# Performance work log

Measured on AMD Instinct MI355X. Metric: run time of the kernel, lower is better.

Reference implementation:

```python
import jax, jax.numpy as jnp
import numpy as np

R = 16                      # grid resolution per axis -> R**3 = 4096 experts
E = R ** 3
L_XYZ = 10                  # xyz positional-encoding frequencies -> input_ch = 63
L_DIR = 4                   # dir positional-encoding frequencies -> input_ch_views = 27
HID = 32                    # KiloNeRF W
AABB_MIN = -1.5
AABB_MAX = 1.5


def posenc(x, L):
    # NeRF positional encoding: [x, sin(2^l x), cos(2^l x)] for l in 0..L-1
    freqs = 2.0 ** jnp.arange(L, dtype=x.dtype)          # (L,)
    xb = x[..., None, :] * freqs[:, None]                # (..., L, 3)
    enc = jnp.concatenate([jnp.sin(xb), jnp.cos(xb)], axis=-1)  # (..., L, 6)
    return jnp.concatenate([x, enc.reshape(x.shape[:-1] + (-1,))], axis=-1)


def _linear_init(key, shape, fan_in):
    s = 1.0 / np.sqrt(fan_in)
    return jax.random.uniform(key, shape, jnp.float32, -s, s)


def setup_inputs() -> dict:
    key = jax.random.key(0)
    ks = jax.random.split(key, 16)
    in_pts = 3 + 6 * L_XYZ     # 63
    in_dirs = 3 + 6 * L_DIR    # 27
    in_view = in_dirs + HID    # 59
    return {
        "pts": jax.random.normal(ks[0], (1024, 64, 3), jnp.float32),
        "viewdirs": jax.random.normal(ks[1], (1024, 3), jnp.float32),
        "W1": _linear_init(ks[2], (E, in_pts, HID), in_pts),
        "b1": _linear_init(ks[3], (E, HID), in_pts),
        "W2": _linear_init(ks[4], (E, HID, HID), HID),
        "b2": _linear_init(ks[5], (E, HID), HID),
        "Wf": _linear_init(ks[6], (E, HID, HID), HID),
        "bf": _linear_init(ks[7], (E, HID), HID),
        "Wsig": _linear_init(ks[8], (E, HID, 1), HID),
        "bsig": _linear_init(ks[9], (E, 1), HID),
        "Wv": _linear_init(ks[10], (E, in_view, HID), in_view),
        "bv": _linear_init(ks[11], (E, HID), in_view),
        "Wrgb": _linear_init(ks[12], (E, HID, 3), HID),
        "brgb": _linear_init(ks[13], (E, 3), HID),
    }


def reference(pts, viewdirs, W1, b1, W2, b2, Wf, bf, Wsig, bsig, Wv, bv, Wrgb, brgb):
    N_rays, N_samples, _ = pts.shape
    p = pts.reshape(-1, 3)                                           # (N,3)
    d = jnp.broadcast_to(viewdirs[:, None, :], (N_rays, N_samples, 3)).reshape(-1, 3)

    # voxel index per point (Network._get_index)
    norm = (p - AABB_MIN) / (AABB_MAX - AABB_MIN)
    scaled = jnp.clip(norm * R, 0.0, R - 1.0)
    idx = scaled.astype(jnp.int32)                                   # (N,3)
    e = idx[:, 0] * (R * R) + idx[:, 1] * R + idx[:, 2]              # (N,) expert id

    xp = posenc(p, L_XYZ)                                            # (N,63)
    xd = posenc(d, L_DIR)                                            # (N,27)

    # grouped tiny-MLP dispatch, vectorized as per-point gathered weights
    h = jax.nn.relu(jnp.einsum('ni,nio->no', xp, W1[e]) + b1[e])     # (N,32)
    h = jax.nn.relu(jnp.einsum('ni,nio->no', h, W2[e]) + b2[e])      # (N,32)
    sigma = jnp.einsum('ni,nio->no', h, Wsig[e]) + bsig[e]           # (N,1)
    feat = jnp.einsum('ni,nio->no', h, Wf[e]) + bf[e]                # (N,32)
    hv = jnp.concatenate([feat, xd], axis=-1)                        # (N,59)
    hv = jax.nn.relu(jnp.einsum('ni,nio->no', hv, Wv[e]) + bv[e])    # (N,32)
    rgb = jnp.einsum('ni,nio->no', hv, Wrgb[e]) + brgb[e]            # (N,3)

    return rgb.reshape(N_rays, N_samples, 3), sigma.reshape(N_rays, N_samples, 1)
```

## Files before the change

### kernel.cpp

```cpp
#include <hip/hip_runtime.h>


#define WS_COUNTS 0
#define WS_OFFSETS 4096
#define WS_CURSOR 8192
#define WS_ORDER 12288

#define L_W1 0
#define L_W2 2016
#define L_WF 3040
#define L_WV 4064
#define L_WS 5952
#define L_WR 5984
#define L_B1 6080
#define L_B2 6112
#define L_BF 6144
#define L_BV 6176
#define L_BSR 6208
#define L_TOT 6212

__device__ __forceinline__ int expert_id(float px, float py, float pz) {
    float nx = (px - (-1.5f)) / 3.0f;
    float ny = (py - (-1.5f)) / 3.0f;
    float nz = (pz - (-1.5f)) / 3.0f;
    float sx = fminf(fmaxf(nx * 16.0f, 0.0f), 15.0f);
    float sy = fminf(fmaxf(ny * 16.0f, 0.0f), 15.0f);
    float sz = fminf(fmaxf(nz * 16.0f, 0.0f), 15.0f);
    return (int)sx * 256 + (int)sy * 16 + (int)sz;
}

template <int N4>
__device__ __forceinline__ void stage256(float* dst, const float* __restrict__ src,
                                         int tid) {
    constexpr int ITER = (N4 + 255) / 256;
    float4 buf[ITER];
#pragma unroll
    for (int j = 0; j < ITER; ++j) {
        const int t = j * 256 + tid;
        if (t < N4) buf[j] = ((const float4*)src)[t];
    }
#pragma unroll
    for (int j = 0; j < ITER; ++j) {
        const int t = j * 256 + tid;
        if (t < N4) ((float4*)dst)[t] = buf[j];
    }
}

__device__ __forceinline__ float enc_val(int idx, float x, float y, float z) {
    if (idx < 3) return (idx == 0) ? x : ((idx == 1) ? y : z);
    const int k = idx - 3;
    const int l = k / 6;
    const int r = k - 6 * l;
    const int c = (r < 3) ? r : r - 3;
    const float cv = (c == 0) ? x : ((c == 1) ? y : z);
    const float a = ldexpf(cv, l);
    return (r < 3) ? sinf(a) : cosf(a);
}

__global__ __launch_bounds__(256) void hist_kernel(const float* __restrict__ pts,
                                                   int* __restrict__ counts, int n) {
    int i = blockIdx.x * 256 + threadIdx.x;
    if (i < n) {
        int e = expert_id(pts[3 * i + 0], pts[3 * i + 1], pts[3 * i + 2]);
        atomicAdd(&counts[e], 1);
    }
}

__global__ __launch_bounds__(256) void scan_kernel(const int* __restrict__ counts,
                                                   int* __restrict__ offsets,
                                                   int* __restrict__ cursor) {
    const int tid = threadIdx.x;
    const int lane = tid & 63, wave = tid >> 6;
    const int base = tid * 16;
    int c[16], loc[16], sum = 0;
#pragma unroll
    for (int j = 0; j < 16; ++j) c[j] = counts[base + j];
#pragma unroll
    for (int j = 0; j < 16; ++j) { loc[j] = sum; sum += c[j]; }
    int v = sum;
#pragma unroll
    for (int off = 1; off <= 32; off <<= 1) {
        int u = __shfl_up(v, off, 64);
        if (lane >= off) v += u;
    }
    __shared__ int wtot[4];
    if (lane == 63) wtot[wave] = v;
    __syncthreads();
    int wbase = 0;
    for (int w = 0; w < wave; ++w) wbase += wtot[w];
    const int excl = wbase + v - sum;
#pragma unroll
    for (int j = 0; j < 16; ++j) {
        int o = excl + loc[j];
        offsets[base + j] = o;
        cursor[base + j] = o;
    }
}

__global__ __launch_bounds__(256) void scatter_kernel(const float* __restrict__ pts,
                                                      int* __restrict__ cursor,
                                                      int* __restrict__ order, int n) {
    int i = blockIdx.x * 256 + threadIdx.x;
    if (i < n) {
        int e = expert_id(pts[3 * i + 0], pts[3 * i + 1], pts[3 * i + 2]);
        int pos = atomicAdd(&cursor[e], 1);
        order[pos] = i;
    }
}

__global__ __launch_bounds__(256) void expert_mlp_kernel(
    const float* __restrict__ pts, const float* __restrict__ viewdirs,
    const float* __restrict__ W1, const float* __restrict__ b1,
    const float* __restrict__ W2, const float* __restrict__ b2,
    const float* __restrict__ Wf, const float* __restrict__ bfc,
    const float* __restrict__ Wsig, const float* __restrict__ bsig,
    const float* __restrict__ Wv, const float* __restrict__ bv,
    const float* __restrict__ Wrgb, const float* __restrict__ brgb,
    const int* __restrict__ counts, const int* __restrict__ offsets,
    const int* __restrict__ order,
    float* __restrict__ out_rgb, float* __restrict__ out_sigma, int samples) {

    const int e = blockIdx.x;
    const int cnt = counts[e];
    if (cnt == 0) return;
    const int start = offsets[e];
    const int tid = threadIdx.x;
    const int wave = tid >> 6;
    const int lane = tid & 63;
    const int h = lane >> 5;
    const int o = lane & 31;

    __shared__ float lw[L_TOT];
    __shared__ float xs[4][4][64];
    __shared__ float xd[4][4][32];

    stage256<504>(lw + L_W1, W1 + (size_t)e * 2016, tid);
    stage256<256>(lw + L_W2, W2 + (size_t)e * 1024, tid);
    stage256<256>(lw + L_WF, Wf + (size_t)e * 1024, tid);
    stage256<472>(lw + L_WV, Wv + (size_t)e * 1888, tid);
    stage256<8>(lw + L_WS, Wsig + (size_t)e * 32, tid);
    stage256<24>(lw + L_WR, Wrgb + (size_t)e * 96, tid);
    stage256<8>(lw + L_B1, b1 + (size_t)e * 32, tid);
    stage256<8>(lw + L_B2, b2 + (size_t)e * 32, tid);
    stage256<8>(lw + L_BF, bfc + (size_t)e * 32, tid);
    stage256<8>(lw + L_BV, bv + (size_t)e * 32, tid);
    if (tid == 0) lw[L_BSR] = bsig[e];
    if (tid < 3) lw[L_BSR + 1 + tid] = brgb[3 * e + tid];
    __syncthreads();

    const float b1o = lw[L_B1 + o];
    const float b2o = lw[L_B2 + o];
    const float bfo = lw[L_BF + o];
    const float bvo = lw[L_BV + o];
    const float wsg = lw[L_WS + o];
    const float wr0 = lw[L_WR + 3 * o + 0];
    const float wr1 = lw[L_WR + 3 * o + 1];
    const float wr2 = lw[L_WR + 3 * o + 2];
    const float bsg = lw[L_BSR];
    const float br0 = lw[L_BSR + 1], br1 = lw[L_BSR + 2], br2 = lw[L_BSR + 3];

    float* xsA = xs[wave][h];     float* xsB = xs[wave][2 + h];
    float* xdA = xd[wave][h];     float* xdB = xd[wave][2 + h];

    const bool pow2 = (samples & (samples - 1)) == 0;
    const int sh = 31 - __clz(samples);

    for (int s0 = 4 * wave; s0 < cnt; s0 += 16) {
        const int sA = s0 + h, sB = s0 + 2 + h;
        const bool liveA = (sA < cnt), liveB = (sB < cnt);
        const int ptA = order[start + (liveA ? sA : cnt - 1)];
        const int ptB = order[start + (liveB ? sB : cnt - 1)];

        const float pxA = pts[3 * ptA + 0], pyA = pts[3 * ptA + 1], pzA = pts[3 * ptA + 2];
        const float pxB = pts[3 * ptB + 0], pyB = pts[3 * ptB + 1], pzB = pts[3 * ptB + 2];
        const int rayA = pow2 ? (ptA >> sh) : (ptA / samples);
        const int rayB = pow2 ? (ptB >> sh) : (ptB / samples);
        const float dxA = viewdirs[3 * rayA + 0], dyA = viewdirs[3 * rayA + 1], dzA = viewdirs[3 * rayA + 2];
        const float dxB = viewdirs[3 * rayB + 0], dyB = viewdirs[3 * rayB + 1], dzB = viewdirs[3 * rayB + 2];

        xsA[o] = enc_val(o, pxA, pyA, pzA);
        xsB[o] = enc_val(o, pxB, pyB, pzB);
        if (o < 31) {
            xsA[o + 32] = enc_val(o + 32, pxA, pyA, pzA);
            xsB[o + 32] = enc_val(o + 32, pxB, pyB, pzB);
        }
        if (o < 27) {
            xdA[o] = enc_val(o, dxA, dyA, dzA);
            xdB[o] = enc_val(o, dxB, dyB, dzB);
        }

        float aA = b1o, aB = b1o;
#pragma unroll
        for (int q = 0; q < 15; ++q) {
            const float w0 = lw[L_W1 + (4 * q + 0) * 32 + o];
            const float w1 = lw[L_W1 + (4 * q + 1) * 32 + o];
            const float w2 = lw[L_W1 + (4 * q + 2) * 32 + o];
            const float w3 = lw[L_W1 + (4 * q + 3) * 32 + o];
            const float4 xA = *(const float4*)&xsA[4 * q];
            const float4 xB = *(const float4*)&xsB[4 * q];
            aA = fmaf(xA.x, w0, aA); aB = fmaf(xB.x, w0, aB);
            aA = fmaf(xA.y, w1, aA); aB = fmaf(xB.y, w1, aB);
            aA = fmaf(xA.z, w2, aA); aB = fmaf(xB.z, w2, aB);
            aA = fmaf(xA.w, w3, aA); aB = fmaf(xB.w, w3, aB);
        }
#pragma unroll
        for (int i = 60; i < 63; ++i) {
            const float w = lw[L_W1 + i * 32 + o];
            aA = fmaf(xsA[i], w, aA); aB = fmaf(xsB[i], w, aB);
        }
        xsA[o] = fmaxf(aA, 0.f);
        xsB[o] = fmaxf(aB, 0.f);

        aA = b2o; aB = b2o;
#pragma unroll
        for (int q = 0; q < 8; ++q) {
            const float w0 = lw[L_W2 + (4 * q + 0) * 32 + o];
            const float w1 = lw[L_W2 + (4 * q + 1) * 32 + o];
            const float w2 = lw[L_W2 + (4 * q + 2) * 32 + o];
            const float w3 = lw[L_W2 + (4 * q + 3) * 32 + o];
            const float4 xA = *(const float4*)&xsA[4 * q];
            const float4 xB = *(const float4*)&xsB[4 * q];
            aA = fmaf(xA.x, w0, aA); aB = fmaf(xB.x, w0, aB);
            aA = fmaf(xA.y, w1, aA); aB = fmaf(xB.y, w1, aB);
            aA = fmaf(xA.z, w2, aA); aB = fmaf(xB.z, w2, aB);
            aA = fmaf(xA.w, w3, aA); aB = fmaf(xB.w, w3, aB);
        }
        const float gA = fmaxf(aA, 0.f), gB = fmaxf(aB, 0.f);

        {
            float spA = gA * wsg, spB = gB * wsg;
#pragma unroll
            for (int m = 1; m <= 16; m <<= 1) {
                spA += __shfl_xor(spA, m, 64);
                spB += __shfl_xor(spB, m, 64);
            }
            if (liveA && o == 0) out_sigma[ptA] = spA + bsg;
            if (liveB && o == 0) out_sigma[ptB] = spB + bsg;
        }
        xsA[o] = gA;
        xsB[o] = gB;

        aA = bfo; aB = bfo;
#pragma unroll
        for (int q = 0; q < 8; ++q) {
            const float w0 = lw[L_WF + (4 * q + 0) * 32 + o];
            const float w1 = lw[L_WF + (4 * q + 1) * 32 + o];
            const float w2 = lw[L_WF + (4 * q + 2) * 32 + o];
            const float w3 = lw[L_WF + (4 * q + 3) * 32 + o];
            const float4 xA = *(const float4*)&xsA[4 * q];
            const float4 xB = *(const float4*)&xsB[4 * q];
            aA = fmaf(xA.x, w0, aA); aB = fmaf(xB.x, w0, aB);
            aA = fmaf(xA.y, w1, aA); aB = fmaf(xB.y, w1, aB);
            aA = fmaf(xA.z, w2, aA); aB = fmaf(xB.z, w2, aB);
            aA = fmaf(xA.w, w3, aA); aB = fmaf(xB.w, w3, aB);
        }
        xsA[o] = aA;
        xsB[o] = aB;

        float avA = bvo, avB = bvo;
#pragma unroll
        for (int q = 0; q < 8; ++q) {
            const float w0 = lw[L_WV + (4 * q + 0) * 32 + o];
            const float w1 = lw[L_WV + (4 * q + 1) * 32 + o];
            const float w2 = lw[L_WV + (4 * q + 2) * 32 + o];
            const float w3 = lw[L_WV + (4 * q + 3) * 32 + o];
            const float4 xA = *(const float4*)&xsA[4 * q];
            const float4 xB = *(const float4*)&xsB[4 * q];
            avA = fmaf(xA.x, w0, avA); avB = fmaf(xB.x, w0, avB);
            avA = fmaf(xA.y, w1, avA); avB = fmaf(xB.y, w1, avB);
            avA = fmaf(xA.z, w2, avA); avB = fmaf(xB.z, w2, avB);
            avA = fmaf(xA.w, w3, avA); avB = fmaf(xB.w, w3, avB);
        }
#pragma unroll
        for (int q = 0; q < 6; ++q) {
            const float w0 = lw[L_WV + (32 + 4 * q + 0) * 32 + o];
            const float w1 = lw[L_WV + (32 + 4 * q + 1) * 32 + o];
            const float w2 = lw[L_WV + (32 + 4 * q + 2) * 32 + o];
            const float w3 = lw[L_WV + (32 + 4 * q + 3) * 32 + o];
            const float4 xA = *(const float4*)&xdA[4 * q];
            const float4 xB = *(const float4*)&xdB[4 * q];
            avA = fmaf(xA.x, w0, avA); avB = fmaf(xB.x, w0, avB);
            avA = fmaf(xA.y, w1, avA); avB = fmaf(xB.y, w1, avB);
            avA = fmaf(xA.z, w2, avA); avB = fmaf(xB.z, w2, avB);
            avA = fmaf(xA.w, w3, avA); avB = fmaf(xB.w, w3, avB);
        }
#pragma unroll
        for (int i = 24; i < 27; ++i) {
            const float w = lw[L_WV + (32 + i) * 32 + o];
            avA = fmaf(xdA[i], w, avA); avB = fmaf(xdB[i], w, avB);
        }
        const float hvA = fmaxf(avA, 0.f), hvB = fmaxf(avB, 0.f);

        {
            float r0A = hvA * wr0, r1A = hvA * wr1, r2A = hvA * wr2;
            float r0B = hvB * wr0, r1B = hvB * wr1, r2B = hvB * wr2;
#pragma unroll
            for (int m = 1; m <= 16; m <<= 1) {
                r0A += __shfl_xor(r0A, m, 64);
                r1A += __shfl_xor(r1A, m, 64);
                r2A += __shfl_xor(r2A, m, 64);
                r0B += __shfl_xor(r0B, m, 64);
                r1B += __shfl_xor(r1B, m, 64);
                r2B += __shfl_xor(r2B, m, 64);
            }
            if (liveA && o == 0) {
                out_rgb[3 * ptA + 0] = r0A + br0;
                out_rgb[3 * ptA + 1] = r1A + br1;
                out_rgb[3 * ptA + 2] = r2A + br2;
            }
            if (liveB && o == 0) {
                out_rgb[3 * ptB + 0] = r0B + br0;
                out_rgb[3 * ptB + 1] = r1B + br1;
                out_rgb[3 * ptB + 2] = r2B + br2;
            }
        }
    }
}

extern "C" void kernel_launch(void* const* d_in, const int* in_sizes, int n_in,
                              void* d_out, int out_size, void* d_ws, size_t ws_size,
                              hipStream_t stream) {
    const float* pts      = (const float*)d_in[0];
    const float* viewdirs = (const float*)d_in[1];
    const float* W1   = (const float*)d_in[2];
    const float* b1   = (const float*)d_in[3];
    const float* W2   = (const float*)d_in[4];
    const float* b2   = (const float*)d_in[5];
    const float* Wf   = (const float*)d_in[6];
    const float* bfc  = (const float*)d_in[7];
    const float* Wsig = (const float*)d_in[8];
    const float* bsig = (const float*)d_in[9];
    const float* Wv   = (const float*)d_in[10];
    const float* bv   = (const float*)d_in[11];
    const float* Wrgb = (const float*)d_in[12];
    const float* brgb = (const float*)d_in[13];

    const int n = in_sizes[0] / 3;
    const int n_rays = in_sizes[1] / 3;
    const int samples = n / n_rays;

    float* out_rgb = (float*)d_out;
    float* out_sigma = out_rgb + (size_t)n * 3;

    int* ws = (int*)d_ws;
    int* counts = ws + WS_COUNTS;
    int* offsets = ws + WS_OFFSETS;
    int* cursor = ws + WS_CURSOR;
    int* order = ws + WS_ORDER;

    hipMemsetAsync(counts, 0, 4096 * sizeof(int), stream);
    hist_kernel<<<(n + 255) / 256, 256, 0, stream>>>(pts, counts, n);
    scan_kernel<<<1, 256, 0, stream>>>(counts, offsets, cursor);
    scatter_kernel<<<(n + 255) / 256, 256, 0, stream>>>(pts, cursor, order, n);
    expert_mlp_kernel<<<4096, 256, 0, stream>>>(
        pts, viewdirs, W1, b1, W2, b2, Wf, bfc, Wsig, bsig, Wv, bv, Wrgb, brgb,
        counts, offsets, order, out_rgb, out_sigma, samples);
}
```

Measured before the change: 258.2 us.

## Aggregate expert atomics per wave and process four samples per half-wave

```diff
diff --git a/kernel.cpp b/kernel.cpp
--- a/kernel.cpp
+++ b/kernel.cpp
@@ -59,10 +59,18 @@
 
 __global__ __launch_bounds__(256) void hist_kernel(const float* __restrict__ pts,
                                                    int* __restrict__ counts, int n) {
-    int i = blockIdx.x * 256 + threadIdx.x;
-    if (i < n) {
-        int e = expert_id(pts[3 * i + 0], pts[3 * i + 1], pts[3 * i + 2]);
-        atomicAdd(&counts[e], 1);
+    const int i = blockIdx.x * 256 + threadIdx.x;
+    const int lane = threadIdx.x & 63;
+    const bool valid = (i < n);
+    int e = 0;
+    if (valid) e = expert_id(pts[3 * i + 0], pts[3 * i + 1], pts[3 * i + 2]);
+    unsigned long long todo = __ballot(valid);
+    while (todo) {
+        const int leader = __ffsll((unsigned long long)todo) - 1;
+        const int e0 = __shfl(e, leader, 64);
+        const unsigned long long same = __ballot(valid && (e == e0)) & todo;
+        if (lane == leader) atomicAdd(&counts[e0], (int)__popcll(same));
+        todo &= ~same;
     }
 }
 
@@ -100,11 +108,24 @@
 __global__ __launch_bounds__(256) void scatter_kernel(const float* __restrict__ pts,
                                                       int* __restrict__ cursor,
                                                       int* __restrict__ order, int n) {
-    int i = blockIdx.x * 256 + threadIdx.x;
-    if (i < n) {
-        int e = expert_id(pts[3 * i + 0], pts[3 * i + 1], pts[3 * i + 2]);
-        int pos = atomicAdd(&cursor[e], 1);
-        order[pos] = i;
+    const int i = blockIdx.x * 256 + threadIdx.x;
+    const int lane = threadIdx.x & 63;
+    const bool valid = (i < n);
+    int e = 0;
+    if (valid) e = expert_id(pts[3 * i + 0], pts[3 * i + 1], pts[3 * i + 2]);
+    unsigned long long todo = __ballot(valid);
+    while (todo) {
+        const int leader = __ffsll((unsigned long long)todo) - 1;
+        const int e0 = __shfl(e, leader, 64);
+        const unsigned long long same = __ballot(valid && (e == e0)) & todo;
+        int base = 0;
+        if (lane == leader) base = atomicAdd(&cursor[e0], (int)__popcll(same));
+        base = __shfl(base, leader, 64);
+        if (valid && (e == e0)) {
+            const int rank = (int)__popcll(same & ((1ull << lane) - 1ull));
+            order[base + rank] = i;
+        }
+        todo &= ~same;
     }
 }
 
@@ -131,8 +152,8 @@
     const int o = lane & 31;
 
     __shared__ float lw[L_TOT];
-    __shared__ float xs[4][4][64];
-    __shared__ float xd[4][4][32];
+    __shared__ float xs[4][8][64];
+    __shared__ float xd[4][8][32];
 
     stage256<504>(lw + L_W1, W1 + (size_t)e * 2016, tid);
     stage256<256>(lw + L_W2, W2 + (size_t)e * 1024, tid);
@@ -160,36 +181,52 @@
     const float br0 = lw[L_BSR + 1], br1 = lw[L_BSR + 2], br2 = lw[L_BSR + 3];
 
     float* xsA = xs[wave][h];     float* xsB = xs[wave][2 + h];
+    float* xsC = xs[wave][4 + h]; float* xsD = xs[wave][6 + h];
     float* xdA = xd[wave][h];     float* xdB = xd[wave][2 + h];
+    float* xdC = xd[wave][4 + h]; float* xdD = xd[wave][6 + h];
 
     const bool pow2 = (samples & (samples - 1)) == 0;
     const int sh = 31 - __clz(samples);
 
-    for (int s0 = 4 * wave; s0 < cnt; s0 += 16) {
-        const int sA = s0 + h, sB = s0 + 2 + h;
-        const bool liveA = (sA < cnt), liveB = (sB < cnt);
-        const int ptA = order[start + (liveA ? sA : cnt - 1)];
-        const int ptB = order[start + (liveB ? sB : cnt - 1)];
-
-        const float pxA = pts[3 * ptA + 0], pyA = pts[3 * ptA + 1], pzA = pts[3 * ptA + 2];
-        const float pxB = pts[3 * ptB + 0], pyB = pts[3 * ptB + 1], pzB = pts[3 * ptB + 2];
+    for (int s0 = 8 * wave; s0 < cnt; s0 += 32) {
+        const int sA = s0 + h, sB = s0 + 2 + h, sC = s0 + 4 + h, sD = s0 + 6 + h;
+        const bool lA = (sA < cnt), lB = (sB < cnt), lC = (sC < cnt), lD = (sD < cnt);
+        const int ptA = order[start + (lA ? sA : cnt - 1)];
+        const int ptB = order[start + (lB ? sB : cnt - 1)];
+        const int ptC = order[start + (lC ? sC : cnt - 1)];
+        const int ptD = order[start + (lD ? sD : cnt - 1)];
+
+        const float pxA = pts[3 * ptA], pyA = pts[3 * ptA + 1], pzA = pts[3 * ptA + 2];
+        const float pxB = pts[3 * ptB], pyB = pts[3 * ptB + 1], pzB = pts[3 * ptB + 2];
+        const float pxC = pts[3 * ptC], pyC = pts[3 * ptC + 1], pzC = pts[3 * ptC + 2];
+        const float pxD = pts[3 * ptD], pyD = pts[3 * ptD + 1], pzD = pts[3 * ptD + 2];
         const int rayA = pow2 ? (ptA >> sh) : (ptA / samples);
         const int rayB = pow2 ? (ptB >> sh) : (ptB / samples);
-        const float dxA = viewdirs[3 * rayA + 0], dyA = viewdirs[3 * rayA + 1], dzA = viewdirs[3 * rayA + 2];
-        const float dxB = viewdirs[3 * rayB + 0], dyB = viewdirs[3 * rayB + 1], dzB = viewdirs[3 * rayB + 2];
+        const int rayC = pow2 ? (ptC >> sh) : (ptC / samples);
+        const int rayD = pow2 ? (ptD >> sh) : (ptD / samples);
+        const float dxA = viewdirs[3 * rayA], dyA = viewdirs[3 * rayA + 1], dzA = viewdirs[3 * rayA + 2];
+        const float dxB = viewdirs[3 * rayB], dyB = viewdirs[3 * rayB + 1], dzB = viewdirs[3 * rayB + 2];
+        const float dxC = viewdirs[3 * rayC], dyC = viewdirs[3 * rayC + 1], dzC = viewdirs[3 * rayC + 2];
+        const float dxD = viewdirs[3 * rayD], dyD = viewdirs[3 * rayD + 1], dzD = viewdirs[3 * rayD + 2];
 
         xsA[o] = enc_val(o, pxA, pyA, pzA);
         xsB[o] = enc_val(o, pxB, pyB, pzB);
+        xsC[o] = enc_val(o, pxC, pyC, pzC);
+        xsD[o] = enc_val(o, pxD, pyD, pzD);
         if (o < 31) {
             xsA[o + 32] = enc_val(o + 32, pxA, pyA, pzA);
             xsB[o + 32] = enc_val(o + 32, pxB, pyB, pzB);
+            xsC[o + 32] = enc_val(o + 32, pxC, pyC, pzC);
+            xsD[o + 32] = enc_val(o + 32, pxD, pyD, pzD);
         }
         if (o < 27) {
             xdA[o] = enc_val(o, dxA, dyA, dzA);
             xdB[o] = enc_val(o, dxB, dyB, dzB);
-        }
-
-        float aA = b1o, aB = b1o;
+            xdC[o] = enc_val(o, dxC, dyC, dzC);
+            xdD[o] = enc_val(o, dxD, dyD, dzD);
+        }
+
+        float aA = b1o, aB = b1o, aC = b1o, aD = b1o;
 #pragma unroll
         for (int q = 0; q < 15; ++q) {
             const float w0 = lw[L_W1 + (4 * q + 0) * 32 + o];
@@ -198,20 +235,27 @@
             const float w3 = lw[L_W1 + (4 * q + 3) * 32 + o];
             const float4 xA = *(const float4*)&xsA[4 * q];
             const float4 xB = *(const float4*)&xsB[4 * q];
+            const float4 xC = *(const float4*)&xsC[4 * q];
+            const float4 xD = *(const float4*)&xsD[4 * q];
             aA = fmaf(xA.x, w0, aA); aB = fmaf(xB.x, w0, aB);
+            aC = fmaf(xC.x, w0, aC); aD = fmaf(xD.x, w0, aD);
             aA = fmaf(xA.y, w1, aA); aB = fmaf(xB.y, w1, aB);
+            aC = fmaf(xC.y, w1, aC); aD = fmaf(xD.y, w1, aD);
             aA = fmaf(xA.z, w2, aA); aB = fmaf(xB.z, w2, aB);
+            aC = fmaf(xC.z, w2, aC); aD = fmaf(xD.z, w2, aD);
             aA = fmaf(xA.w, w3, aA); aB = fmaf(xB.w, w3, aB);
+            aC = fmaf(xC.w, w3, aC); aD = fmaf(xD.w, w3, aD);
         }
 #pragma unroll
         for (int i = 60; i < 63; ++i) {
             const float w = lw[L_W1 + i * 32 + o];
             aA = fmaf(xsA[i], w, aA); aB = fmaf(xsB[i], w, aB);
-        }
-        xsA[o] = fmaxf(aA, 0.f);
-        xsB[o] = fmaxf(aB, 0.f);
-
-        aA = b2o; aB = b2o;
+            aC = fmaf(xsC[i], w, aC); aD = fmaf(xsD[i], w, aD);
+        }
+        xsA[o] = fmaxf(aA, 0.f);  xsB[o] = fmaxf(aB, 0.f);
+        xsC[o] = fmaxf(aC, 0.f);  xsD[o] = fmaxf(aD, 0.f);
+
+        aA = b2o; aB = b2o; aC = b2o; aD = b2o;
 #pragma unroll
         for (int q = 0; q < 8; ++q) {
             const float w0 = lw[L_W2 + (4 * q + 0) * 32 + o];
@@ -220,27 +264,39 @@
             const float w3 = lw[L_W2 + (4 * q + 3) * 32 + o];
             const float4 xA = *(const float4*)&xsA[4 * q];
             const float4 xB = *(const float4*)&xsB[4 * q];
+            const float4 xC = *(const float4*)&xsC[4 * q];
+            const float4 xD = *(const float4*)&xsD[4 * q];
             aA = fmaf(xA.x, w0, aA); aB = fmaf(xB.x, w0, aB);
+            aC = fmaf(xC.x, w0, aC); aD = fmaf(xD.x, w0, aD);
             aA = fmaf(xA.y, w1, aA); aB = fmaf(xB.y, w1, aB);
+            aC = fmaf(xC.y, w1, aC); aD = fmaf(xD.y, w1, aD);
             aA = fmaf(xA.z, w2, aA); aB = fmaf(xB.z, w2, aB);
+            aC = fmaf(xC.z, w2, aC); aD = fmaf(xD.z, w2, aD);
             aA = fmaf(xA.w, w3, aA); aB = fmaf(xB.w, w3, aB);
+            aC = fmaf(xC.w, w3, aC); aD = fmaf(xD.w, w3, aD);
         }
         const float gA = fmaxf(aA, 0.f), gB = fmaxf(aB, 0.f);
+        const float gC = fmaxf(aC, 0.f), gD = fmaxf(aD, 0.f);
 
         {
-            float spA = gA * wsg, spB = gB * wsg;
+            float sA2 = gA * wsg, sB2 = gB * wsg, sC2 = gC * wsg, sD2 = gD * wsg;
 #pragma unroll
             for (int m = 1; m <= 16; m <<= 1) {
-                spA += __shfl_xor(spA, m, 64);
-                spB += __shfl_xor(spB, m, 64);
+                sA2 += __shfl_xor(sA2, m, 64);
+                sB2 += __shfl_xor(sB2, m, 64);
+                sC2 += __shfl_xor(sC2, m, 64);
+                sD2 += __shfl_xor(sD2, m, 64);
             }
-            if (liveA && o == 0) out_sigma[ptA] = spA + bsg;
-            if (liveB && o == 0) out_sigma[ptB] = spB + bsg;
-        }
-        xsA[o] = gA;
-        xsB[o] = gB;
-
-        aA = bfo; aB = bfo;
+            if (o == 0) {
+                if (lA) out_sigma[ptA] = sA2 + bsg;
+                if (lB) out_sigma[ptB] = sB2 + bsg;
+                if (lC) out_sigma[ptC] = sC2 + bsg;
+                if (lD) out_sigma[ptD] = sD2 + bsg;
+            }
+        }
+        xsA[o] = gA; xsB[o] = gB; xsC[o] = gC; xsD[o] = gD;
+
+        aA = bfo; aB = bfo; aC = bfo; aD = bfo;
 #pragma unroll
         for (int q = 0; q < 8; ++q) {
             const float w0 = lw[L_WF + (4 * q + 0) * 32 + o];
@@ -249,15 +305,20 @@
             const float w3 = lw[L_WF + (4 * q + 3) * 32 + o];
             const float4 xA = *(const float4*)&xsA[4 * q];
             const float4 xB = *(const float4*)&xsB[4 * q];
+            const float4 xC = *(const float4*)&xsC[4 * q];
+            const float4 xD = *(const float4*)&xsD[4 * q];
             aA = fmaf(xA.x, w0, aA); aB = fmaf(xB.x, w0, aB);
+            aC = fmaf(xC.x, w0, aC); aD = fmaf(xD.x, w0, aD);
             aA = fmaf(xA.y, w1, aA); aB = fmaf(xB.y, w1, aB);
+            aC = fmaf(xC.y, w1, aC); aD = fmaf(xD.y, w1, aD);
             aA = fmaf(xA.z, w2, aA); aB = fmaf(xB.z, w2, aB);
+            aC = fmaf(xC.z, w2, aC); aD = fmaf(xD.z, w2, aD);
             aA = fmaf(xA.w, w3, aA); aB = fmaf(xB.w, w3, aB);
-        }
-        xsA[o] = aA;
-        xsB[o] = aB;
-
-        float avA = bvo, avB = bvo;
+            aC = fmaf(xC.w, w3, aC); aD = fmaf(xD.w, w3, aD);
+        }
+        xsA[o] = aA; xsB[o] = aB; xsC[o] = aC; xsD[o] = aD;
+
+        float vA = bvo, vB = bvo, vC = bvo, vD = bvo;
 #pragma unroll
         for (int q = 0; q < 8; ++q) {
             const float w0 = lw[L_WV + (4 * q + 0) * 32 + o];
@@ -266,10 +327,16 @@
             const float w3 = lw[L_WV + (4 * q + 3) * 32 + o];
             const float4 xA = *(const float4*)&xsA[4 * q];
             const float4 xB = *(const float4*)&xsB[4 * q];
-            avA = fmaf(xA.x, w0, avA); avB = fmaf(xB.x, w0, avB);
-            avA = fmaf(xA.y, w1, avA); avB = fmaf(xB.y, w1, avB);
-            avA = fmaf(xA.z, w2, avA); avB = fmaf(xB.z, w2, avB);
-            avA = fmaf(xA.w, w3, avA); avB = fmaf(xB.w, w3, avB);
+            const float4 xC = *(const float4*)&xsC[4 * q];
+            const float4 xD = *(const float4*)&xsD[4 * q];
+            vA = fmaf(xA.x, w0, vA); vB = fmaf(xB.x, w0, vB);
+            vC = fmaf(xC.x, w0, vC); vD = fmaf(xD.x, w0, vD);
+            vA = fmaf(xA.y, w1, vA); vB = fmaf(xB.y, w1, vB);
+            vC = fmaf(xC.y, w1, vC); vD = fmaf(xD.y, w1, vD);
+            vA = fmaf(xA.z, w2, vA); vB = fmaf(xB.z, w2, vB);
+            vC = fmaf(xC.z, w2, vC); vD = fmaf(xD.z, w2, vD);
+            vA = fmaf(xA.w, w3, vA); vB = fmaf(xB.w, w3, vB);
+            vC = fmaf(xC.w, w3, vC); vD = fmaf(xD.w, w3, vD);
         }
 #pragma unroll
         for (int q = 0; q < 6; ++q) {
@@ -279,39 +346,43 @@
             const float w3 = lw[L_WV + (32 + 4 * q + 3) * 32 + o];
             const float4 xA = *(const float4*)&xdA[4 * q];
             const float4 xB = *(const float4*)&xdB[4 * q];
-            avA = fmaf(xA.x, w0, avA); avB = fmaf(xB.x, w0, avB);
-            avA = fmaf(xA.y, w1, avA); avB = fmaf(xB.y, w1, avB);
-            avA = fmaf(xA.z, w2, avA); avB = fmaf(xB.z, w2, avB);
-            avA = fmaf(xA.w, w3, avA); avB = fmaf(xB.w, w3, avB);
+            const float4 xC = *(const float4*)&xdC[4 * q];
+            const float4 xD = *(const float4*)&xdD[4 * q];
+            vA = fmaf(xA.x, w0, vA); vB = fmaf(xB.x, w0, vB);
+            vC = fmaf(xC.x, w0, vC); vD = fmaf(xD.x, w0, vD);
+            vA = fmaf(xA.y, w1, vA); vB = fmaf(xB.y, w1, vB);
+            vC = fmaf(xC.y, w1, vC); vD = fmaf(xD.y, w1, vD);
+            vA = fmaf(xA.z, w2, vA); vB = fmaf(xB.z, w2, vB);
+            vC = fmaf(xC.z, w2, vC); vD = fmaf(xD.z, w2, vD);
+            vA = fmaf(xA.w, w3, vA); vB = fmaf(xB.w, w3, vB);
+            vC = fmaf(xC.w, w3, vC); vD = fmaf(xD.w, w3, vD);
         }
 #pragma unroll
         for (int i = 24; i < 27; ++i) {
             const float w = lw[L_WV + (32 + i) * 32 + o];
-            avA = fmaf(xdA[i], w, avA); avB = fmaf(xdB[i], w, avB);
-        }
-        const float hvA = fmaxf(avA, 0.f), hvB = fmaxf(avB, 0.f);
+            vA = fmaf(xdA[i], w, vA); vB = fmaf(xdB[i], w, vB);
+            vC = fmaf(xdC[i], w, vC); vD = fmaf(xdD[i], w, vD);
+        }
+        const float hA = fmaxf(vA, 0.f), hB = fmaxf(vB, 0.f);
+        const float hC = fmaxf(vC, 0.f), hD = fmaxf(vD, 0.f);
 
         {
-            float r0A = hvA * wr0, r1A = hvA * wr1, r2A = hvA * wr2;
-            float r0B = hvB * wr0, r1B = hvB * wr1, r2B = hvB * wr2;
+            float r0A = hA * wr0, r1A = hA * wr1, r2A = hA * wr2;
+            float r0B = hB * wr0, r1B = hB * wr1, r2B = hB * wr2;
+            float r0C = hC * wr0, r1C = hC * wr1, r2C = hC * wr2;
+            float r0D = hD * wr0, r1D = hD * wr1, r2D = hD * wr2;
 #pragma unroll
             for (int m = 1; m <= 16; m <<= 1) {
-                r0A += __shfl_xor(r0A, m, 64);
-                r1A += __shfl_xor(r1A, m, 64);
-                r2A += __shfl_xor(r2A, m, 64);
-                r0B += __shfl_xor(r0B, m, 64);
-                r1B += __shfl_xor(r1B, m, 64);
-                r2B += __shfl_xor(r2B, m, 64);
+                r0A += __shfl_xor(r0A, m, 64); r1A += __shfl_xor(r1A, m, 64); r2A += __shfl_xor(r2A, m, 64);
+                r0B += __shfl_xor(r0B, m, 64); r1B += __shfl_xor(r1B, m, 64); r2B += __shfl_xor(r2B, m, 64);
+                r0C += __shfl_xor(r0C, m, 64); r1C += __shfl_xor(r1C, m, 64); r2C += __shfl_xor(r2C, m, 64);
+                r0D += __shfl_xor(r0D, m, 64); r1D += __shfl_xor(r1D, m, 64); r2D += __shfl_xor(r2D, m, 64);
             }
-            if (liveA && o == 0) {
-                out_rgb[3 * ptA + 0] = r0A + br0;
-                out_rgb[3 * ptA + 1] = r1A + br1;
-                out_rgb[3 * ptA + 2] = r2A + br2;
-            }
-            if (liveB && o == 0) {
-                out_rgb[3 * ptB + 0] = r0B + br0;
-                out_rgb[3 * ptB + 1] = r1B + br1;
-                out_rgb[3 * ptB + 2] = r2B + br2;
+            if (o == 0) {
+                if (lA) { out_rgb[3 * ptA] = r0A + br0; out_rgb[3 * ptA + 1] = r1A + br1; out_rgb[3 * ptA + 2] = r2A + br2; }
+                if (lB) { out_rgb[3 * ptB] = r0B + br0; out_rgb[3 * ptB + 1] = r1B + br1; out_rgb[3 * ptB + 2] = r2B + br2; }
+                if (lC) { out_rgb[3 * ptC] = r0C + br0; out_rgb[3 * ptC + 1] = r1C + br1; out_rgb[3 * ptC + 2] = r2C + br2; }
+                if (lD) { out_rgb[3 * ptD] = r0D + br0; out_rgb[3 * ptD + 1] = r1D + br1; out_rgb[3 * ptD + 2] = r2D + br2; }
             }
         }
     }
```

After: 278.6 us. +7.9%, slower.
